# Optimization experiments

Measured on AMD Instinct MI355X. Metric: run time of the kernel, lower is better.

Reference implementation:

```python
import jax, jax.numpy as jnp
import numpy as np

N_NODE = 4096
K = 32           # num_nearest_neighbors
HIDDEN = 128
RMS_EPS = 1e-5
DT = 0.01        # init scale for linear weights (init_linear_weights(..., scale=dt))


def _rmsnorm(x, g):
    # RMSNorm over last dim with learned scale (eqx.nn.RMSNorm-style)
    return x * jax.lax.rsqrt(jnp.mean(x * x, axis=-1, keepdims=True) + RMS_EPS) * g


def _pos_mlp(x, W1, b1, g1, W2, b2, g2, W3, b3):
    # MLPWithLayerNorm(in=2, width=HIDDEN, depth=2, out=1, act=silu, rms_norm=True):
    # per hidden layer: Linear -> RMSNorm -> SiLU; final Linear with identity activation.
    h = jax.nn.silu(_rmsnorm(x @ W1.T + b1, g1))
    h = jax.nn.silu(_rmsnorm(h @ W2.T + b2, g2))
    return h @ W3.T + b3  # [E, 1]


def setup_inputs() -> dict:
    key = jax.random.key(0)
    ks = jax.random.split(key, 8)

    def xavier(k, shape):
        fan_in, fan_out = shape[1], shape[0]
        std = jnp.sqrt(2.0 / (fan_in + fan_out))
        return (jax.random.normal(k, shape, dtype=jnp.float32) * std * DT)

    return {
        "pos": jax.random.normal(ks[0], (N_NODE, 3), dtype=jnp.float32),
        "t": jax.random.uniform(ks[1], (1,), dtype=jnp.float32),
        "W1": xavier(ks[2], (HIDDEN, 2)),
        "b1": jnp.zeros((HIDDEN,), dtype=jnp.float32),
        "g1": jnp.ones((HIDDEN,), dtype=jnp.float32),
        "W2": xavier(ks[3], (HIDDEN, HIDDEN)),
        "b2": jnp.zeros((HIDDEN,), dtype=jnp.float32),
        "g2": jnp.ones((HIDDEN,), dtype=jnp.float32),
        "W3": xavier(ks[4], (1, HIDDEN)),
        "b3": jnp.zeros((1,), dtype=jnp.float32),
    }


def reference(pos, t, W1, b1, g1, W2, b2, g2, W3, b3):
    n = pos.shape[0]
    # Pairwise squared distances for kNN graph build
    diff = pos[:, None, :] - pos[None, :, :]              # [n, n, 3]
    radial_full = jnp.sum(diff * diff, axis=-1)           # [n, n]
    masked = radial_full.at[jnp.diag_indices(n)].set(jnp.inf)
    _, recv = jax.lax.top_k(-masked, k=K)                 # [n, K] nearest neighbors
    senders = jnp.repeat(jnp.arange(n), K)                # [n*K]
    receivers = recv.reshape(-1)                          # [n*K]

    # Gather edge geometry (normalize=False)
    coord_diff = pos[senders] - pos[receivers]            # [E, 3]
    radial = jnp.sum(coord_diff * coord_diff, axis=1, keepdims=True)  # [E, 1]

    # Per-edge MLP on [radial, t]
    t_scalar = jnp.reshape(t, ())
    edge_features = jnp.concatenate(
        [radial, jnp.full_like(radial, t_scalar)], axis=-1)          # [E, 2]
    edge_scalars = _pos_mlp(edge_features, W1, b1, g1, W2, b2, g2, W3, b3).squeeze(-1)

    # Scatter-sum messages back to sender nodes, average by neighbor count
    trans = coord_diff * edge_scalars[:, None]            # [E, 3]
    seg_sum = jax.ops.segment_sum(trans, senders, num_segments=n)    # [n, 3]
    seg_count = jnp.maximum(float(K), 1.0)
    return pos + seg_sum / seg_count
```

## Files before the change

kernel.cpp:

```cpp
#include <hip/hip_runtime.h>
#include <stdint.h>

#define NN   4096
#define KK   32
#define HID  128
#define BLK  256
#define WPB  4
#define GRID (NN / WPB)
#define CAP  128

typedef unsigned short bf16_t;
typedef __attribute__((ext_vector_type(8))) short bf16x8;
typedef __attribute__((ext_vector_type(4))) float f32x4;

#define FINF __uint_as_float(0x7f800000u)

__device__ __forceinline__ bf16_t f2bf(float f) {
    uint32_t u = __float_as_uint(f);
    u = u + 0x7fffu + ((u >> 16) & 1u);
    return (bf16_t)(u >> 16);
}
__device__ __forceinline__ float siluf(float x) {
    return x / (1.0f + __expf(-x));
}

__device__ __forceinline__ void dist4(const float4* __restrict__ p4, int g, int lane,
                                      float px, float py, float pz, int iself,
                                      float d[4]) {
    float4 f0 = p4[g*192 + 3*lane];
    float4 f1 = p4[g*192 + 3*lane + 1];
    float4 f2 = p4[g*192 + 3*lane + 2];
    float jx[4] = {f0.x, f0.w, f1.z, f2.y};
    float jy[4] = {f0.y, f1.x, f1.w, f2.z};
    float jz[4] = {f0.z, f1.y, f2.x, f2.w};
    #pragma unroll
    for (int c = 0; c < 4; ++c) {
        int j = g*256 + 4*lane + c;
        float dx = px - jx[c], dy = py - jy[c], dz = pz - jz[c];
        float dd = __fadd_rn(__fadd_rn(__fmul_rn(dx,dx), __fmul_rn(dy,dy)),
                             __fmul_rn(dz,dz));
        d[c] = (j == iself) ? FINF : dd;
    }
}

__global__ __launch_bounds__(256) void prepack_w2(
    const float* __restrict__ W2, uint4* __restrict__ w2b)
{
    int c  = blockIdx.x * 256 + threadIdx.x;
    int f  = c >> 6, ln = c & 63;
    int NT = f >> 2, kk = f & 3;
    int row = NT*16 + (ln & 15);
    int k0  = kk*32 + (ln >> 4) * 8;
    const float* s = W2 + row * HID + k0;
    float4 lo = *(const float4*)s;
    float4 hi = *(const float4*)(s + 4);
    uint4 pk;
    pk.x = (uint32_t)f2bf(lo.x) | ((uint32_t)f2bf(lo.y) << 16);
    pk.y = (uint32_t)f2bf(lo.z) | ((uint32_t)f2bf(lo.w) << 16);
    pk.z = (uint32_t)f2bf(hi.x) | ((uint32_t)f2bf(hi.y) << 16);
    pk.w = (uint32_t)f2bf(hi.z) | ((uint32_t)f2bf(hi.w) << 16);
    w2b[c] = pk;
}

template<bool WS>
struct __align__(16) Sm {
    ushort   h1[WPB][KK * HID];
    uint32_t cand[WPB][CAP];
    float    rads[WPB][KK];
    float    sedge[WPB][KK];
    int      recvs[WPB][KK];
    int      cnt[WPB];
    uint32_t w2l[WS ? 4 : HID * 64];
};

template<bool WS>
__global__ __launch_bounds__(BLK) void egnn_main(
    const float* __restrict__ pos, const float* __restrict__ tptr,
    const float* __restrict__ W1,  const float* __restrict__ b1,
    const float* __restrict__ g1,  const float* __restrict__ W2,
    const float* __restrict__ b2,  const float* __restrict__ g2,
    const float* __restrict__ W3,  const float* __restrict__ b3,
    const uint4* __restrict__ w2b, float* __restrict__ out)
{
    __shared__ Sm<WS> sm;
    const int tid  = threadIdx.x;
    const int lane = tid & 63;
    const int wid  = tid >> 6;
    const int i    = blockIdx.x * WPB + wid;
    const int l15  = lane & 15, lq = lane >> 4;

    const float ts  = tptr[0];
    const float b3s = b3[0];

    float A2, AC, C2;
    {
        const float4 w1v = ((const float4*)W1)[lane];
        const float2 b1v = ((const float2*)b1)[lane];
        float t0 = ts * w1v.y + b1v.x;
        float t1 = ts * w1v.w + b1v.y;
        A2 = w1v.x*w1v.x + w1v.z*w1v.z;
        AC = w1v.x*t0    + w1v.z*t1;
        C2 = t0*t0       + t1*t1;
        #pragma unroll
        for (int m = 32; m >= 1; m >>= 1) {
            A2 += __shfl_xor(A2, m, 64);
            AC += __shfl_xor(AC, m, 64);
            C2 += __shfl_xor(C2, m, 64);
        }
    }

    if constexpr (!WS) {
        for (int idx = tid; idx < HID * 16; idx += BLK) {
            int row = idx >> 4, c = idx & 15;
            const float* src = W2 + row * HID + c * 8;
            float4 lo = *(const float4*)src;
            float4 hi = *(const float4*)(src + 4);
            uint4 pk;
            pk.x = (uint32_t)f2bf(lo.x) | ((uint32_t)f2bf(lo.y) << 16);
            pk.y = (uint32_t)f2bf(lo.z) | ((uint32_t)f2bf(lo.w) << 16);
            pk.z = (uint32_t)f2bf(hi.x) | ((uint32_t)f2bf(hi.y) << 16);
            pk.w = (uint32_t)f2bf(hi.z) | ((uint32_t)f2bf(hi.w) << 16);
            *((uint4*)&sm.w2l[row * 64 + 4 * (c ^ (row & 15))]) = pk;
        }
        __syncthreads();
    }

    if (lane == 0) sm.cnt[wid] = 0;

    const float px = pos[3*i], py = pos[3*i+1], pz = pos[3*i+2];
    const float4* p4 = (const float4*)pos;

    float mind = FINF;
    for (int g = 0; g < 16; ++g) {
        float d[4];
        dist4(p4, g, lane, px, py, pz, i, d);
        mind = fminf(fminf(fminf(mind, d[0]), fminf(d[1], d[2])), d[3]);
    }
    const uint32_t m16 = __float_as_uint(mind) >> 16;

    uint32_t v = 0;
    #pragma unroll
    for (int b = 15; b >= 0; --b) {
        uint32_t t = v | (1u << b);
        int nl = (int)__popcll(__ballot(m16 < t));
        if (nl < KK) v = t;
    }

    for (int g = 0; g < 16; ++g) {
        float d[4];
        dist4(p4, g, lane, px, py, pz, i, d);
        #pragma unroll
        for (int c = 0; c < 4; ++c) {
            uint32_t d16 = __float_as_uint(d[c]) >> 16;
            if (d16 <= v) {
                int slot = atomicAdd(&sm.cnt[wid], 1);
                if (slot < CAP)
                    sm.cand[wid][slot] = (d16 << 16) | (unsigned)(g*256 + 4*lane + c);
            }
        }
    }
    const int cntv = sm.cnt[wid];

    if (cntv <= CAP) {
        #pragma unroll
        for (int h = 0; h < 2; ++h) {
            int idx = h*64 + lane;
            if (idx < cntv) {
                uint32_t km = sm.cand[wid][idx];
                int rank = 0;
                for (int q = 0; q < cntv; q += 4) {
                    uint4 u = *((const uint4*)&sm.cand[wid][q]);
                    rank += (q     < cntv && u.x < km) ? 1 : 0;
                    rank += (q + 1 < cntv && u.y < km) ? 1 : 0;
                    rank += (q + 2 < cntv && u.z < km) ? 1 : 0;
                    rank += (q + 3 < cntv && u.w < km) ? 1 : 0;
                }
                if (rank < KK) sm.recvs[wid][rank] = (int)(km & 0xFFFFu);
            }
        }
    } else {
        unsigned long long locmask = 0ull;
        for (int it = 0; it < KK; ++it) {
            unsigned long long best = ~0ull;
            for (int g = 0; g < 16; ++g) {
                float d[4];
                dist4(p4, g, lane, px, py, pz, i, d);
                #pragma unroll
                for (int c = 0; c < 4; ++c) {
                    bool dead = ((locmask >> (g*4 + c)) & 1ull) != 0ull;
                    unsigned long long key = dead ? ~0ull
                        : ((((unsigned long long)__float_as_uint(d[c])) << 12)
                           | (unsigned)(g*256 + 4*lane + c));
                    best = best < key ? best : key;
                }
            }
            #pragma unroll
            for (int m = 32; m >= 1; m >>= 1) {
                unsigned long long o = __shfl_xor(best, m, 64);
                best = best < o ? best : o;
            }
            int j = (int)(best & 0xfffull);
            if (lane == 0) sm.recvs[wid][it] = j;
            if (((j >> 2) & 63) == lane)
                locmask |= 1ull << ((j >> 8) * 4 + (j & 3));
        }
    }

    float cdx = 0.f, cdy = 0.f, cdz = 0.f;
    if (lane < KK) {
        int r = sm.recvs[wid][lane];
        cdx = px - pos[3*r];
        cdy = py - pos[3*r+1];
        cdz = pz - pos[3*r+2];
        float rad = __fadd_rn(__fadd_rn(__fmul_rn(cdx,cdx), __fmul_rn(cdy,cdy)),
                              __fmul_rn(cdz,cdz));
        sm.rads[wid][lane] = rad;
    }

    {
        const int ch = lane >> 2, epr = lane & 3;
        float4 wA = ((const float4*)W1)[ch*4    ];
        float4 wB = ((const float4*)W1)[ch*4 + 1];
        float4 wC = ((const float4*)W1)[ch*4 + 2];
        float4 wD = ((const float4*)W1)[ch*4 + 3];
        float4 bA = ((const float4*)b1)[ch*2], bB = ((const float4*)b1)[ch*2 + 1];
        float4 gA = ((const float4*)g1)[ch*2], gB = ((const float4*)g1)[ch*2 + 1];
        float av[8] = {wA.x, wA.z, wB.x, wB.z, wC.x, wC.z, wD.x, wD.z};
        float cv[8] = {ts*wA.y + bA.x, ts*wA.w + bA.y, ts*wB.y + bA.z, ts*wB.w + bA.w,
                       ts*wC.y + bB.x, ts*wC.w + bB.y, ts*wD.y + bB.z, ts*wD.w + bB.w};
        float gv[8] = {gA.x, gA.y, gA.z, gA.w, gB.x, gB.y, gB.z, gB.w};
        uint4* h1q = (uint4*)&sm.h1[wid][0];
        #pragma unroll
        for (int g = 0; g < 8; ++g) {
            int E = 4*g + epr;
            float rad = sm.rads[wid][E];
            float sqv = rad*rad*A2 + 2.0f*rad*AC + C2;
            float rn  = rsqrtf(sqv * (1.0f/HID) + 1e-5f);
            uint32_t pk[4];
            #pragma unroll
            for (int p = 0; p < 4; ++p) {
                float va = siluf((rad*av[2*p]   + cv[2*p])   * rn * gv[2*p]);
                float vb = siluf((rad*av[2*p+1] + cv[2*p+1]) * rn * gv[2*p+1]);
                pk[p] = (__float_as_uint(va) >> 16) | (__float_as_uint(vb) & 0xffff0000u);
            }
            h1q[E*16 + (ch ^ (E & 15))] = uint4{pk[0], pk[1], pk[2], pk[3]};
        }
    }

    float g2v[8], w3v[8], b2v[8];
    #pragma unroll
    for (int nt = 0; nt < 8; ++nt) {
        int n = nt*16 + l15;
        g2v[nt] = g2[n]; w3v[nt] = W3[n]; b2v[nt] = b2[n];
    }

    const bf16x8* h1v = (const bf16x8*)&sm.h1[wid][0];
    #pragma unroll
    for (int mt = 0; mt < 2; ++mt) {
        f32x4 acc[8];
        #pragma unroll
        for (int nt = 0; nt < 8; ++nt) acc[nt] = f32x4{0.f, 0.f, 0.f, 0.f};
        const int m = mt*16 + l15;
        if constexpr (WS) {
            const bf16x8* bv = (const bf16x8*)w2b;
            #pragma unroll
            for (int kk = 0; kk < 4; ++kk) {
                bf16x8 af = h1v[m*16 + ((kk*4 + lq) ^ l15)];
                #pragma unroll
                for (int nt = 0; nt < 8; ++nt)
                    acc[nt] = __builtin_amdgcn_mfma_f32_16x16x32_bf16(
                                  af, bv[(nt*4 + kk)*64 + lane], acc[nt], 0, 0, 0);
            }
        } else {
            const bf16x8* w2v = (const bf16x8*)sm.w2l;
            #pragma unroll
            for (int kk = 0; kk < 4; ++kk) {
                const int q = (kk*4 + lq) ^ l15;
                bf16x8 af = h1v[m*16 + q];
                #pragma unroll
                for (int nt = 0; nt < 8; ++nt)
                    acc[nt] = __builtin_amdgcn_mfma_f32_16x16x32_bf16(
                                  af, w2v[(nt*16 + l15)*16 + q], acc[nt], 0, 0, 0);
            }
        }

        float ss[4];
        #pragma unroll
        for (int r = 0; r < 4; ++r) {
            float t = 0.f;
            #pragma unroll
            for (int nt = 0; nt < 8; ++nt) {
                float zz = acc[nt][r] + b2v[nt];
                acc[nt][r] = zz;
                t += zz*zz;
            }
            ss[r] = t;
        }
        #pragma unroll
        for (int m2 = 1; m2 <= 8; m2 <<= 1) {
            #pragma unroll
            for (int r = 0; r < 4; ++r) ss[r] += __shfl_xor(ss[r], m2, 64);
        }
        float sp[4];
        #pragma unroll
        for (int r = 0; r < 4; ++r) {
            float rn = rsqrtf(ss[r] * (1.0f/HID) + 1e-5f);
            float t = 0.f;
            #pragma unroll
            for (int nt = 0; nt < 8; ++nt)
                t += siluf(acc[nt][r] * rn * g2v[nt]) * w3v[nt];
            sp[r] = t;
        }
        #pragma unroll
        for (int m2 = 1; m2 <= 8; m2 <<= 1) {
            #pragma unroll
            for (int r = 0; r < 4; ++r) sp[r] += __shfl_xor(sp[r], m2, 64);
        }
        if (l15 == 0) {
            #pragma unroll
            for (int r = 0; r < 4; ++r)
                sm.sedge[wid][mt*16 + lq*4 + r] = sp[r] + b3s;
        }
    }

    float mx = 0.f, my = 0.f, mz = 0.f;
    if (lane < KK) {
        float s = sm.sedge[wid][lane];
        mx = cdx * s; my = cdy * s; mz = cdz * s;
    }
    #pragma unroll
    for (int m = 32; m >= 1; m >>= 1) {
        mx += __shfl_xor(mx, m, 64);
        my += __shfl_xor(my, m, 64);
        mz += __shfl_xor(mz, m, 64);
    }
    if (lane == 0) {
        out[3*i    ] = px + mx * (1.0f/KK);
        out[3*i + 1] = py + my * (1.0f/KK);
        out[3*i + 2] = pz + mz * (1.0f/KK);
    }
}

extern "C" void kernel_launch(void* const* d_in, const int* in_sizes, int n_in,
                              void* d_out, int out_size, void* d_ws, size_t ws_size,
                              hipStream_t stream) {
    (void)in_sizes; (void)n_in; (void)out_size;
    const float* pos = (const float*)d_in[0];
    const float* t   = (const float*)d_in[1];
    const float* W1  = (const float*)d_in[2];
    const float* b1  = (const float*)d_in[3];
    const float* g1  = (const float*)d_in[4];
    const float* W2  = (const float*)d_in[5];
    const float* b2  = (const float*)d_in[6];
    const float* g2  = (const float*)d_in[7];
    const float* W3  = (const float*)d_in[8];
    const float* b3  = (const float*)d_in[9];
    float* out = (float*)d_out;

    if (d_ws != nullptr && ws_size >= 32768) {
        prepack_w2<<<8, 256, 0, stream>>>(W2, (uint4*)d_ws);
        egnn_main<true><<<GRID, BLK, 0, stream>>>(
            pos, t, W1, b1, g1, W2, b2, g2, W3, b3, (const uint4*)d_ws, out);
    } else {
        egnn_main<false><<<GRID, BLK, 0, stream>>>(
            pos, t, W1, b1, g1, W2, b2, g2, W3, b3, nullptr, out);
    }
}
```

Baseline: 120.9 us.

## Cache truncated distances in shared memory and compact candidates with ballot prefix

The first distance pass now stores each truncated 16-bit distance in a per-wave shared buffer, which is unioned with the h1 tile. The second pass reads those values back instead of recomputing distances from global positions. The shared-memory atomicAdd for candidate slots is replaced by a wave ballot with a popcount prefix, which makes slot assignment deterministic and ordered. This trades extra shared-memory writes and reads for removing the repeated global loads, the distance arithmetic and the atomic contention.

```diff
diff --git a/kernel.cpp b/kernel.cpp
--- a/kernel.cpp
+++ b/kernel.cpp
@@ -64,12 +64,14 @@
 
 template<bool WS>
 struct __align__(16) Sm {
-    ushort   h1[WPB][KK * HID];
+    union __align__(16) U {
+        ushort dbf[NN];
+        ushort h1[KK * HID];
+    } uw[WPB];
     uint32_t cand[WPB][CAP];
     float    rads[WPB][KK];
     float    sedge[WPB][KK];
     int      recvs[WPB][KK];
-    int      cnt[WPB];
     uint32_t w2l[WS ? 4 : HID * 64];
 };
 
@@ -125,16 +127,21 @@
         __syncthreads();
     }
 
-    if (lane == 0) sm.cnt[wid] = 0;
-
     const float px = pos[3*i], py = pos[3*i+1], pz = pos[3*i+2];
     const float4* p4 = (const float4*)pos;
 
     float mind = FINF;
-    for (int g = 0; g < 16; ++g) {
-        float d[4];
-        dist4(p4, g, lane, px, py, pz, i, d);
-        mind = fminf(fminf(fminf(mind, d[0]), fminf(d[1], d[2])), d[3]);
+    {
+        ushort* dbf = sm.uw[wid].dbf;
+        #pragma unroll 4
+        for (int g = 0; g < 16; ++g) {
+            float d[4];
+            dist4(p4, g, lane, px, py, pz, i, d);
+            uint32_t lo = (__float_as_uint(d[0]) >> 16) | (__float_as_uint(d[1]) & 0xffff0000u);
+            uint32_t hi = (__float_as_uint(d[2]) >> 16) | (__float_as_uint(d[3]) & 0xffff0000u);
+            *((uint2*)&dbf[g*256 + 4*lane]) = make_uint2(lo, hi);
+            mind = fminf(fminf(fminf(mind, d[0]), fminf(d[1], d[2])), d[3]);
+        }
     }
     const uint32_t m16 = __float_as_uint(mind) >> 16;
 
@@ -146,20 +153,28 @@
         if (nl < KK) v = t;
     }
 
-    for (int g = 0; g < 16; ++g) {
-        float d[4];
-        dist4(p4, g, lane, px, py, pz, i, d);
-        #pragma unroll
-        for (int c = 0; c < 4; ++c) {
-            uint32_t d16 = __float_as_uint(d[c]) >> 16;
-            if (d16 <= v) {
-                int slot = atomicAdd(&sm.cnt[wid], 1);
-                if (slot < CAP)
-                    sm.cand[wid][slot] = (d16 << 16) | (unsigned)(g*256 + 4*lane + c);
-            }
-        }
-    }
-    const int cntv = sm.cnt[wid];
+    uint32_t cnt = 0;
+    {
+        const ushort* dbf = sm.uw[wid].dbf;
+        const unsigned long long below = (1ull << lane) - 1ull;
+        for (int g = 0; g < 16; ++g) {
+            uint2 w = *((const uint2*)&dbf[g*256 + 4*lane]);
+            uint32_t d16v[4] = {w.x & 0xffffu, w.x >> 16, w.y & 0xffffu, w.y >> 16};
+            #pragma unroll
+            for (int c = 0; c < 4; ++c) {
+                bool pred = d16v[c] <= v;
+                unsigned long long mb = __ballot(pred);
+                if (pred) {
+                    int slot = (int)cnt + (int)__popcll(mb & below);
+                    if (slot < CAP)
+                        sm.cand[wid][slot] = (d16v[c] << 16)
+                                           | (unsigned)(g*256 + 4*lane + c);
+                }
+                cnt += (uint32_t)__popcll(mb);
+            }
+        }
+    }
+    const int cntv = (int)cnt;
 
     if (cntv <= CAP) {
         #pragma unroll
@@ -229,7 +244,7 @@
         float cv[8] = {ts*wA.y + bA.x, ts*wA.w + bA.y, ts*wB.y + bA.z, ts*wB.w + bA.w,
                        ts*wC.y + bB.x, ts*wC.w + bB.y, ts*wD.y + bB.z, ts*wD.w + bB.w};
         float gv[8] = {gA.x, gA.y, gA.z, gA.w, gB.x, gB.y, gB.z, gB.w};
-        uint4* h1q = (uint4*)&sm.h1[wid][0];
+        uint4* h1q = (uint4*)&sm.uw[wid].h1[0];
         #pragma unroll
         for (int g = 0; g < 8; ++g) {
             int E = 4*g + epr;
@@ -254,7 +269,7 @@
         g2v[nt] = g2[n]; w3v[nt] = W3[n]; b2v[nt] = b2[n];
     }
 
-    const bf16x8* h1v = (const bf16x8*)&sm.h1[wid][0];
+    const bf16x8* h1v = (const bf16x8*)&sm.uw[wid].h1[0];
     #pragma unroll
     for (int mt = 0; mt < 2; ++mt) {
         f32x4 acc[8];
```

Measured after the change: 114.5 us. 5.2% less time.
